# Kernel optimization log

Measured on AMD Instinct MI355X. Metric: run time of the kernel, lower is better.

## Reference

```python
import jax, jax.numpy as jnp
import numpy as np

HID = 1024
RATIO = 4          # compress_ratio
SELECT_K = 512
WINDOW = 256
N_HEADS = 16
SCALE = 1.0 / np.sqrt(HID // N_HEADS)  # 1/sqrt(head_size), head_size=64


def setup_inputs() -> dict:
    key = jax.random.key(0)
    ks = jax.random.split(key, 12)
    std = 0.02
    d = {
        "hidden_states": jax.random.normal(ks[0], (4, 4096, HID), jnp.float32),
        # torch Linear weight [out,in] stored here transposed as [in,out]
        "Wq": jax.random.normal(ks[1], (HID, HID), jnp.float32) * std,
        "bq": jnp.zeros((HID,), jnp.float32),
        "Wk": jax.random.normal(ks[2], (HID, HID), jnp.float32) * std,
        "bk": jnp.zeros((HID,), jnp.float32),
        "Wv": jax.random.normal(ks[3], (HID, HID), jnp.float32) * std,
        "bv": jnp.zeros((HID,), jnp.float32),
        "Wo": jax.random.normal(ks[4], (3 * HID, HID), jnp.float32) * std,
        "bo": jnp.zeros((HID,), jnp.float32),
        "Wg": jax.random.normal(ks[5], (HID, 3), jnp.float32) * std,
        "bg": jnp.zeros((3,), jnp.float32),
        "Wc": jax.random.normal(ks[6], (RATIO * HID, HID), jnp.float32) * std,
        "bc": jnp.zeros((HID,), jnp.float32),
        "Ws": jax.random.normal(ks[7], (HID, 1), jnp.float32) * std,
        "bs": jnp.zeros((1,), jnp.float32),
    }
    return d


def _adjust(t, L):
    cur = t.shape[1]
    if cur < L:
        return jnp.pad(t, ((0, 0), (0, L - cur), (0, 0)))
    return t[:, :L]


def _attend(x, Wq, bq, Wk, bk, Wv, bv):
    # x: [..., T, H]; full single-head attention over axis -2
    q = x @ Wq + bq
    k = x @ Wk + bk
    v = x @ Wv + bv
    s = jnp.einsum('...qd,...kd->...qk', q, k) * SCALE
    p = jax.nn.softmax(s, axis=-1)
    return jnp.einsum('...qk,...kd->...qd', p, v)


def reference(hidden_states, Wq, bq, Wk, bk, Wv, bv, Wo, bo, Wg, bg, Wc, bc, Ws, bs):
    B, L, H = hidden_states.shape

    # --- gates ---
    gates = jax.nn.sigmoid(hidden_states @ Wg + bg)
    gates = gates / (gates.sum(-1, keepdims=True) + 1e-6)

    # --- compress branch: block-compress then full attention over blocks ---
    pad_c = (-L) % RATIO
    xc = jnp.pad(hidden_states, ((0, 0), (0, pad_c), (0, 0)))
    blocks = xc.reshape(B, -1, RATIO * H)
    compressed = blocks @ Wc + bc                      # [B, Lc, H]
    comp_out = _adjust(_attend(compressed, Wq, bq, Wk, bk, Wv, bv), L)

    # --- select branch: top-k token gather then full attention ---
    k_eff = min(SELECT_K, L)
    scores = (hidden_states @ Ws + bs)[..., 0]         # [B, L]
    _, idx = jax.lax.top_k(scores, k_eff)
    idx = jnp.sort(idx, axis=-1)
    selected = jnp.take_along_axis(hidden_states, idx[..., None], axis=1)  # [B, k, H]
    sel_out = _adjust(_attend(selected, Wq, bq, Wk, bk, Wv, bv), L)

    # --- window branch: overlapping sliding windows (stride W/2) ---
    W = min(WINDOW, L)
    pad_w = (-L) % W
    xw = jnp.pad(hidden_states, ((0, 0), (0, pad_w), (0, 0)))
    Lp = xw.shape[1]
    starts = np.arange(0, Lp - W + 1, W // 2)
    widx = starts[:, None] + np.arange(W)              # [nw, W] static
    win = xw[:, widx]                                   # [B, nw, W, H]
    win_ctx = _attend(win, Wq, bq, Wk, bk, Wv, bv)      # [B, nw, W, H]
    win_out = _adjust(win_ctx.reshape(B, -1, H), L)

    # --- gated combine + output projection + residual + layernorm ---
    combined = jnp.concatenate([
        comp_out * gates[..., 0:1],
        sel_out * gates[..., 1:2],
        win_out * gates[..., 2:3],
    ], axis=-1)
    out = combined @ Wo + bo
    out = out * 0.5 + hidden_states * 0.5
    mu = out.mean(-1, keepdims=True)
    var = out.var(-1, keepdims=True)
    return (out - mu) * jax.lax.rsqrt(var + 1e-6)
```

## Files before the change

### kernel.cpp

```cpp
#include <hip/hip_runtime.h>
#include <hip/hip_bf16.h>

typedef __bf16 bf16;
typedef __bf16 bf16x4 __attribute__((ext_vector_type(4)));
typedef __bf16 bf16x8 __attribute__((ext_vector_type(8)));
typedef float floatx4 __attribute__((ext_vector_type(4)));

#define MFMA16(a, b, c) __builtin_amdgcn_mfma_f32_16x16x32_bf16((a), (b), (c), 0, 0, 0)
#define SCALE_F 0.125f

#define GLDS(gp, lp) __builtin_amdgcn_global_load_lds( \
    (const __attribute__((address_space(1))) void*)(gp), \
    (__attribute__((address_space(3))) void*)(lp), 16, 0, 0)

__global__ __launch_bounds__(256) void prep_kernel(const float* __restrict__ Wq, const float* __restrict__ Wk,
                                                   const float* __restrict__ Wv, const float* __restrict__ Wo,
                                                   const float* __restrict__ Wc,
                                                   const float* __restrict__ bq, const float* __restrict__ bk,
                                                   const float* __restrict__ bv,
                                                   bf16* __restrict__ wqkvT, bf16* __restrict__ woT,
                                                   bf16* __restrict__ wcT, float* __restrict__ bqkv) {
    const int z = blockIdx.z;
    const int tx = threadIdx.x, ty = threadIdx.y;
    if (z == 10) {
        int bid = blockIdx.y * 32 + blockIdx.x;
        if (bid < 12) {
            int i = bid * 256 + ty * 32 + tx;
            float v = (i < 1024) ? bq[i] : (i < 2048 ? bk[i - 1024] : bv[i - 2048]);
            bqkv[i] = v;
        }
        return;
    }
    __shared__ float tile[32][33];
    const float* in;
    bf16* out;
    int R;
    if (z < 3)      { in = (z == 0 ? Wq : (z == 1 ? Wk : Wv)); out = wqkvT + (size_t)z * 1048576; R = 1024; }
    else if (z < 6) { in = Wo + (size_t)(z - 3) * 1048576; out = woT + (size_t)(z - 3) * 1048576; R = 1024; }
    else            { in = Wc + (size_t)(z - 6) * 1048576; out = wcT + (z - 6) * 1024; R = 4096; }
    int bx = blockIdx.x * 32, by = blockIdx.y * 32;
#pragma unroll
    for (int i = 0; i < 32; i += 8)
        tile[ty + i][tx] = in[(size_t)(by + ty + i) * 1024 + bx + tx];
    __syncthreads();
#pragma unroll
    for (int i = 0; i < 32; i += 8)
        out[(size_t)(bx + ty + i) * R + by + tx] = (bf16)tile[tx][ty + i];
}

__global__ __launch_bounds__(256) void gates_scores_kernel(const float* __restrict__ x,
                                                           const float* __restrict__ Wg, const float* __restrict__ bg,
                                                           const float* __restrict__ Ws, const float* __restrict__ bs,
                                                           float* __restrict__ gates, float* __restrict__ scores,
                                                           bf16* __restrict__ xb) {
    int row = blockIdx.x * 4 + (threadIdx.x >> 6);
    int lane = threadIdx.x & 63;
    const float* xr = x + (size_t)row * 1024 + lane * 16;
    float g0 = 0.f, g1 = 0.f, g2 = 0.f;
    double sc = 0.0;
    bf16x8 xo0, xo1;
#pragma unroll
    for (int i = 0; i < 16; i++) {
        float xv = xr[i];
        if (i < 8) xo0[i] = (bf16)xv; else xo1[i - 8] = (bf16)xv;
        int k = lane * 16 + i;
        g0 += xv * Wg[k * 3 + 0];
        g1 += xv * Wg[k * 3 + 1];
        g2 += xv * Wg[k * 3 + 2];
        sc += (double)(xv * Ws[k]);
    }
    bf16* xbp = xb + (size_t)row * 1024 + lane * 16;
    *(bf16x8*)xbp = xo0;
    *(bf16x8*)(xbp + 8) = xo1;
    for (int off = 1; off < 64; off <<= 1) {
        g0 += __shfl_xor(g0, off);
        g1 += __shfl_xor(g1, off);
        g2 += __shfl_xor(g2, off);
        sc += __shfl_xor(sc, off);
    }
    if (lane == 0) {
        g0 = 1.0f / (1.0f + __expf(-(g0 + bg[0])));
        g1 = 1.0f / (1.0f + __expf(-(g1 + bg[1])));
        g2 = 1.0f / (1.0f + __expf(-(g2 + bg[2])));
        float den = g0 + g1 + g2 + 1e-6f;
        gates[(size_t)row * 3 + 0] = g0 / den;
        gates[(size_t)row * 3 + 1] = g1 / den;
        gates[(size_t)row * 3 + 2] = g2 / den;
        scores[row] = (float)(sc + (double)bs[0]);
    }
}

__global__ __launch_bounds__(256) void rank_kernel(const float* __restrict__ scores, int* __restrict__ rankP) {
    __shared__ float s[1024];
    const int b = blockIdx.z, jc = blockIdx.y;
    const int i = blockIdx.x * 256 + threadIdx.x;
    const float* sb = scores + b * 4096;
    ((float4*)s)[threadIdx.x] = ((const float4*)(sb + jc * 1024))[threadIdx.x];
    __syncthreads();
    const float si = sb[i];
    const int jbase = jc * 1024;
    int cnt = 0;
#pragma unroll 4
    for (int jj = 0; jj < 1024; jj += 4) {
        float4 v = *(const float4*)(s + jj);
        int j0 = jbase + jj;
        cnt += (v.x > si) || (v.x == si && (j0 + 0) < i);
        cnt += (v.y > si) || (v.y == si && (j0 + 1) < i);
        cnt += (v.z > si) || (v.z == si && (j0 + 2) < i);
        cnt += (v.w > si) || (v.w == si && (j0 + 3) < i);
    }
    rankP[jc * 16384 + b * 4096 + i] = cnt;
}

__global__ __launch_bounds__(1024) void select_kernel(const int* __restrict__ rankP, int* __restrict__ sidx) {
    __shared__ int psum[1024];
    int b = blockIdx.x, t = threadIdx.x;
    const int* rb = rankP + b * 4096;
    int f[4];
#pragma unroll
    for (int k = 0; k < 4; k++) {
        int idx = 4 * t + k;
        int r = rb[idx] + rb[16384 + idx] + rb[32768 + idx] + rb[49152 + idx];
        f[k] = r < 512;
    }
    psum[t] = f[0] + f[1] + f[2] + f[3];
    __syncthreads();
    for (int off = 1; off < 1024; off <<= 1) {
        int u = (t >= off) ? psum[t - off] : 0;
        __syncthreads();
        psum[t] += u;
        __syncthreads();
    }
    int pos = t ? psum[t - 1] : 0;
    int* ob = sidx + b * 512;
    if (f[0]) ob[pos++] = 4 * t + 0;
    if (f[1]) ob[pos++] = 4 * t + 1;
    if (f[2]) ob[pos++] = 4 * t + 2;
    if (f[3]) ob[pos++] = 4 * t + 3;
}

__global__ __launch_bounds__(256) void gather_kernel(const bf16* __restrict__ Qf, const bf16* __restrict__ Kf,
                                                     const bf16* __restrict__ Vf, const int* __restrict__ sidx,
                                                     bf16* __restrict__ sq, bf16* __restrict__ sk,
                                                     bf16* __restrict__ sv) {
    int e = blockIdx.x * 256 + threadIdx.x;
    int col = (e & 127) * 8;
    int i = (e >> 7) & 511;
    int b = e >> 16;
    int src = b * 4096 + (sidx[b * 512 + i] & 4095);
    size_t so = (size_t)src * 1024 + col;
    size_t dofs = (size_t)(b * 512 + i) * 1024 + col;
    *(float4*)(sq + dofs) = *(const float4*)(Qf + so);
    *(float4*)(sk + dofs) = *(const float4*)(Kf + so);
    *(float4*)(sv + dofs) = *(const float4*)(Vf + so);
}

__global__ __launch_bounds__(256) void addcvt4_kernel(const float* __restrict__ P0, const float* __restrict__ P1,
                                                      const float* __restrict__ P2, const float* __restrict__ P3,
                                                      const float* __restrict__ bc, bf16* __restrict__ outp) {
    int i = blockIdx.x * 256 + threadIdx.x;
    float4 a = ((const float4*)P0)[i];
    float4 b = ((const float4*)P1)[i];
    float4 c = ((const float4*)P2)[i];
    float4 d = ((const float4*)P3)[i];
    int col = (i << 2) & 1023;
    bf16x4 o;
    o[0] = (bf16)(a.x + b.x + c.x + d.x + bc[col + 0]);
    o[1] = (bf16)(a.y + b.y + c.y + d.y + bc[col + 1]);
    o[2] = (bf16)(a.z + b.z + c.z + d.z + bc[col + 2]);
    o[3] = (bf16)(a.w + b.w + c.w + d.w + bc[col + 3]);
    *(bf16x4*)(outp + ((size_t)i << 2)) = o;
}

template <bool NZF, bool F32OUT, bool ACC, bool REMAP>
__global__ __launch_bounds__(256) void gemm3(const bf16* __restrict__ A, const bf16* __restrict__ Bt,
                                             void* __restrict__ Cv, const float* __restrict__ bias, int biasz,
                                             int K, int lda, int ldb, int ldc, int zdiv,
                                             size_t sAhi, size_t sAlo, size_t sBhi, size_t sBlo,
                                             size_t sChi, size_t sClo, int mpbA, int mpbC) {
    __shared__ float4 smA[512], smB[512];
    bf16* sA = (bf16*)smA;
    bf16* sB = (bf16*)smB;
    const int t = threadIdx.x;
    const int lane = t & 63, quad = lane >> 4, l16 = lane & 15;
    const int wv = t >> 6, wm = wv >> 1, wn = wv & 1;
    const int mt = blockIdx.y;
    int nt, zh, zl;
    if constexpr (NZF) {
        zh = blockIdx.z;
        zl = blockIdx.x / zdiv;
        nt = blockIdx.x - zl * zdiv;
    } else {
        nt = blockIdx.x;
        int z = blockIdx.z;
        zh = z / zdiv;
        zl = z - zh * zdiv;
    }
    A  += (size_t)zh * sAhi + (size_t)zl * sAlo;
    Bt += (size_t)zh * sBhi + (size_t)zl * sBlo;
    const size_t cofs = (size_t)zh * sChi + (size_t)zl * sClo;

    floatx4 acc[4][4] = {};

    const bf16* Ap = A + (size_t)(mt * 128 + (t >> 2)) * lda + (t & 3) * 8;
    const bf16* Bp = Bt + (size_t)(nt * 128 + (t >> 2)) * ldb + (t & 3) * 8;
    const size_t rA = (size_t)64 * lda, rB = (size_t)64 * ldb;
    bf16* lA0 = sA + wv * 512;
    bf16* lA1 = sA + 2048 + wv * 512;
    bf16* lB0 = sB + wv * 512;
    bf16* lB1 = sB + 2048 + wv * 512;

    for (int k0 = 0; k0 < K; k0 += 32) {
        __syncthreads();
        GLDS(Ap + k0,      lA0);
        GLDS(Ap + rA + k0, lA1);
        GLDS(Bp + k0,      lB0);
        GLDS(Bp + rB + k0, lB1);
        __syncthreads();
        bf16x8 af[4], bfr[4];
#pragma unroll
        for (int i = 0; i < 4; i++) af[i] = *(const bf16x8*)(sA + (wm * 64 + i * 16 + l16) * 32 + quad * 8);
#pragma unroll
        for (int j = 0; j < 4; j++) bfr[j] = *(const bf16x8*)(sB + (wn * 64 + j * 16 + l16) * 32 + quad * 8);
#pragma unroll
        for (int i = 0; i < 4; i++)
#pragma unroll
            for (int j = 0; j < 4; j++) acc[i][j] = MFMA16(af[i], bfr[j], acc[i][j]);
    }

#pragma unroll
    for (int i = 0; i < 4; i++) {
        int gr0 = mt * 128 + wm * 64 + i * 16 + quad * 4;
#pragma unroll
        for (int j = 0; j < 4; j++) {
            int gc = nt * 128 + wn * 64 + j * 16 + l16;
            float bvl = bias ? bias[zl * biasz + gc] : 0.0f;
#pragma unroll
            for (int r = 0; r < 4; r++) {
                int row = gr0 + r;
                size_t crow = REMAP ? ((size_t)(row / mpbA) * mpbC + (row % mpbA)) : (size_t)row;
                size_t off = cofs + crow * ldc + gc;
                float v = acc[i][j][r] + bvl;
                if constexpr (F32OUT) {
                    float* Cf = (float*)Cv;
                    if constexpr (ACC) v += Cf[off];
                    Cf[off] = v;
                } else {
                    bf16* Cb = (bf16*)Cv;
                    if constexpr (ACC) v += (float)Cb[off];
                    Cb[off] = (bf16)v;
                }
            }
        }
    }
}

#define BARx()   asm volatile("s_barrier" ::: "memory")
#define LGKM0()  asm volatile("s_waitcnt lgkmcnt(0)" ::: "memory")
#define VMC6()   asm volatile("s_waitcnt vmcnt(6)" ::: "memory")

#define LD_A(bsel, qm) { \
    const bf16* _p = lds + (bsel) * 32768 + (((qm) << 7) + (wm << 6) + l16) * 64; \
    _Pragma("unroll") \
    for (int m = 0; m < 4; m++) { \
        a[m][0] = *(const bf16x8*)(_p + (m << 10) + cg0); \
        a[m][1] = *(const bf16x8*)(_p + (m << 10) + cg1); \
    } }

#define LD_B(bsel, qn) { \
    const bf16* _p = lds + (bsel) * 32768 + 16384 + (((qn) << 7) + (wn << 5) + l16) * 64; \
    _Pragma("unroll") \
    for (int n = 0; n < 2; n++) { \
        b[qn][n][0] = *(const bf16x8*)(_p + (n << 10) + cg0); \
        b[qn][n][1] = *(const bf16x8*)(_p + (n << 10) + cg1); \
    } }

#define ST_A(bsel, h, ko) { \
    bf16* _d = lds + (bsel) * 32768 + (((h) << 7) + (wv << 3)) * 64; \
    const bf16* _g = Ab + (size_t)((h) << 7) * lda + (ko); \
    GLDS(_g, _d); \
    GLDS(_g + ((size_t)lda << 6), _d + 4096); }

#define ST_B(bsel, h, ko) { \
    bf16* _d = lds + (bsel) * 32768 + 16384 + (((h) << 7) + (wv << 3)) * 64; \
    const bf16* _g = Bb + (size_t)((h) << 7) * ldb + (ko); \
    GLDS(_g, _d); \
    GLDS(_g + ((size_t)ldb << 6), _d + 4096); }

#define PH_MMA(qm, qn) { \
    __builtin_amdgcn_s_setprio(1); \
    _Pragma("unroll") \
    for (int kk = 0; kk < 2; kk++) \
    _Pragma("unroll") \
    for (int m = 0; m < 4; m++) \
    _Pragma("unroll") \
    for (int n = 0; n < 2; n++) \
        acc[qm][qn][m][n] = MFMA16(a[m][kk], b[qn][n][kk], acc[qm][qn][m][n]); \
    __builtin_amdgcn_s_setprio(0); }

template <bool NZF, bool F32OUT, bool ACC, bool REMAP>
__global__ __launch_bounds__(512, 2) void gemm256(const bf16* __restrict__ A, const bf16* __restrict__ Bt,
                                                  void* __restrict__ Cv, const float* __restrict__ bias, int biasz,
                                                  int K, int lda, int ldb, int ldc, int zdiv,
                                                  size_t sAhi, size_t sAlo, size_t sBhi, size_t sBlo,
                                                  size_t sChi, size_t sClo, int mpbA, int mpbC) {
    __shared__ float4 ldsv[8192];
    bf16* lds = (bf16*)ldsv;
    const int t = threadIdx.x;
    const int lane = t & 63, quad = lane >> 4, l16 = lane & 15;
    const int wv = t >> 6, wm = wv >> 2, wn = wv & 3;

    const int gx = gridDim.x;
    int lin = blockIdx.x + gx * blockIdx.y;
    const int chunk = (gx * gridDim.y) >> 3;
    lin = (lin & 7) * chunk + (lin >> 3);
    const int bx = lin % gx;
    const int mt = lin / gx;

    int nt, zh, zl;
    if constexpr (NZF) {
        zh = blockIdx.z;
        zl = bx / zdiv;
        nt = bx - zl * zdiv;
    } else {
        nt = bx;
        int z = blockIdx.z;
        zh = z / zdiv;
        zl = z - zh * zdiv;
    }
    A  += (size_t)zh * sAhi + (size_t)zl * sAlo;
    Bt += (size_t)zh * sBhi + (size_t)zl * sBlo;
    const size_t cofs = (size_t)zh * sChi + (size_t)zl * sClo;

    const int srow = (wv << 3) + (lane >> 3);
    const int scol = (((lane & 7) ^ ((lane >> 3) & 7)) << 3);
    const bf16* Ab = A + (size_t)(mt * 256 + srow) * lda + scol;
    const bf16* Bb = Bt + (size_t)(nt * 256 + srow) * ldb + scol;
    const int swz = l16 & 7;
    const int cg0 = ((quad ^ swz) << 3);
    const int cg1 = (((4 | quad) ^ swz) << 3);

    floatx4 acc[2][2][4][2] = {};
    bf16x8 a[4][2], b[2][2][2];

    const int NT = K >> 6;
    ST_A(0, 0, 0);  ST_B(0, 0, 0);  ST_B(0, 1, 0);  ST_A(0, 1, 0);
    ST_A(1, 0, 64); ST_B(1, 0, 64); ST_B(1, 1, 64); ST_A(1, 1, 64);
    VMC6();
    BARx();

#pragma unroll 1
    for (int it = 0; it < (NT >> 1); ++it) {
        const int kt = it << 1;
        const int ko2 = ((kt + 2 < NT) ? kt + 2 : NT - 1) << 6;
        const int ko3 = ((kt + 3 < NT) ? kt + 3 : NT - 1) << 6;
        LD_B(0, 0); LD_A(0, 0);
        PH_MMA(0, 0);
        LGKM0(); BARx();
        LD_B(0, 1);
        ST_A(0, 0, ko2);
        PH_MMA(0, 1);
        LGKM0(); BARx();
        LD_A(0, 1);
        ST_B(0, 0, ko2);
        PH_MMA(1, 1);
        LGKM0(); BARx();
        ST_B(0, 1, ko2);
        PH_MMA(1, 0);
        VMC6(); BARx();
        LD_B(1, 0); LD_A(1, 0);
        ST_A(0, 1, ko2);
        PH_MMA(0, 0);
        LGKM0(); BARx();
        LD_B(1, 1);
        ST_A(1, 0, ko3);
        PH_MMA(0, 1);
        LGKM0(); BARx();
        LD_A(1, 1);
        ST_B(1, 0, ko3);
        PH_MMA(1, 1);
        LGKM0(); BARx();
        ST_B(1, 1, ko3);
        ST_A(1, 1, ko3);
        PH_MMA(1, 0);
        VMC6(); BARx();
    }

    asm volatile("s_waitcnt vmcnt(0)" ::: "memory");
    BARx();

    if constexpr (!ACC && !REMAP) {
        const int STE = F32OUT ? 260 : 264;
        float* ldsf = (float*)ldsv;
        bf16* ldsh = (bf16*)ldsv;
#pragma unroll
        for (int qm = 0; qm < 2; qm++)
#pragma unroll
        for (int mh = 0; mh < 2; mh++) {
#pragma unroll
            for (int qn = 0; qn < 2; qn++)
#pragma unroll
            for (int n = 0; n < 2; n++) {
                const int ccol = qn * 128 + wn * 32 + n * 16 + l16;
                const float bvl = bias ? bias[zl * biasz + nt * 256 + ccol] : 0.0f;
#pragma unroll
                for (int mp = 0; mp < 2; mp++) {
                    const int lr0 = wm * 32 + mp * 16 + quad * 4;
#pragma unroll
                    for (int r = 0; r < 4; r++) {
                        float v = acc[qm][qn][mh * 2 + mp][n][r] + bvl;
                        if constexpr (F32OUT) ldsf[(lr0 + r) * STE + ccol] = v;
                        else                  ldsh[(lr0 + r) * STE + ccol] = (bf16)v;
                    }
                }
            }
            LGKM0(); BARx();
            if constexpr (F32OUT) {
                float* Cf = (float*)Cv;
#pragma unroll
                for (int i = 0; i < 8; i++) {
                    int idx = i * 512 + t;
                    int row = idx >> 6, c4 = (idx & 63) << 2;
                    float4 vv = *(float4*)(ldsf + row * STE + c4);
                    int grow = mt * 256 + qm * 128 + ((row >> 5) << 6) + mh * 32 + (row & 31);
                    *(float4*)(Cf + cofs + (size_t)grow * ldc + nt * 256 + c4) = vv;
                }
            } else {
                bf16* Cb = (bf16*)Cv;
#pragma unroll
                for (int i = 0; i < 4; i++) {
                    int idx = i * 512 + t;
                    int row = idx >> 5, c8 = (idx & 31) << 3;
                    float4 vv = *(float4*)(ldsh + row * STE + c8);
                    int grow = mt * 256 + qm * 128 + ((row >> 5) << 6) + mh * 32 + (row & 31);
                    *(float4*)(Cb + cofs + (size_t)grow * ldc + nt * 256 + c8) = vv;
                }
            }
            LGKM0(); BARx();
        }
    } else {
#pragma unroll
        for (int qm = 0; qm < 2; qm++)
#pragma unroll
        for (int m = 0; m < 4; m++) {
            int gr0 = mt * 256 + qm * 128 + wm * 64 + m * 16 + quad * 4;
#pragma unroll
            for (int qn = 0; qn < 2; qn++)
#pragma unroll
            for (int n = 0; n < 2; n++) {
                int gc = nt * 256 + qn * 128 + wn * 32 + n * 16 + l16;
                float bvl = bias ? bias[zl * biasz + gc] : 0.0f;
#pragma unroll
                for (int r = 0; r < 4; r++) {
                    int row = gr0 + r;
                    size_t crow = REMAP ? ((size_t)(row / mpbA) * mpbC + (row % mpbA)) : (size_t)row;
                    size_t off = cofs + crow * ldc + gc;
                    float v = acc[qm][qn][m][n][r] + bvl;
                    if constexpr (F32OUT) {
                        float* Cf = (float*)Cv;
                        if constexpr (ACC) v += Cf[off];
                        Cf[off] = v;
                    } else {
                        bf16* Cb = (bf16*)Cv;
                        if constexpr (ACC) v += (float)Cb[off];
                        Cb[off] = (bf16)v;
                    }
                }
            }
        }
    }
}

#undef LD_A
#undef LD_B
#undef ST_A
#undef ST_B
#undef PH_MMA

template <int MODE>
__global__ __launch_bounds__(256) void smtb_kernel(const float* __restrict__ S, bf16* __restrict__ P,
                                                   const float* __restrict__ gates, int RL,
                                                   int upb, int wbase, int nsm,
                                                   const bf16* __restrict__ tin, bf16* __restrict__ tout,
                                                   int TR, int TC) {
    __shared__ float red[8];
    __shared__ bf16 tile[32][33];
    const int t = threadIdx.x;
    if ((int)blockIdx.x >= nsm) {
        int tb = blockIdx.x - nsm;
        int bx = (tb & 31) * 32, by = (tb >> 5) * 32;
        int tx = t & 31, ty = t >> 5;
#pragma unroll
        for (int i = 0; i < 32; i += 8)
            tile[ty + i][tx] = tin[(size_t)(by + ty + i) * TC + bx + tx];
        __syncthreads();
#pragma unroll
        for (int i = 0; i < 32; i += 8)
            tout[(size_t)(bx + ty + i) * TR + by + tx] = tile[tx][ty + i];
        return;
    }
    const int row = blockIdx.x;
    const float* srow = S + (size_t)row * RL;
    bf16* prow = P + (size_t)row * RL;
    const int npt = RL >> 8;
    float v[4];
    float m = -1e30f;
    for (int i = 0; i < npt; i++) { v[i] = srow[t + (i << 8)] * SCALE_F; m = fmaxf(m, v[i]); }
    for (int off = 1; off < 64; off <<= 1) m = fmaxf(m, __shfl_xor(m, off));
    const int wvv = t >> 6, lane = t & 63;
    if (lane == 0) red[wvv] = m;
    __syncthreads();
    m = fmaxf(fmaxf(red[0], red[1]), fmaxf(red[2], red[3]));
    float e[4], s = 0.f;
    for (int i = 0; i < npt; i++) { e[i] = __expf(v[i] - m); s += e[i]; }
    for (int off = 1; off < 64; off <<= 1) s += __shfl_xor(s, off);
    if (lane == 0) red[4 + wvv] = s;
    __syncthreads();
    s = red[4] + red[5] + red[6] + red[7];
    int gpos;
    if (MODE == 0)      { gpos = (row >> 10) * 4096 + (row & 1023); }
    else if (MODE == 1) { gpos = (row >> 9) * 4096 + (row & 511); }
    else                { int zz = row >> 8; gpos = (zz / upb) * 4096 + (wbase + zz % upb) * 256 + (row & 255); }
    const float fac = gates[gpos * 3 + MODE] / s;
    for (int i = 0; i < npt; i++) prow[t + (i << 8)] = (bf16)(e[i] * fac);
}

__global__ __launch_bounds__(256) void ln_kernel(float* __restrict__ acc, const float* __restrict__ x) {
    __shared__ float red[8];
    int row = blockIdx.x, t = threadIdx.x;
    float4 a = ((const float4*)(acc + (size_t)row * 1024))[t];
    float4 xv = ((const float4*)(x + (size_t)row * 1024))[t];
    float y[4];
    y[0] = 0.5f * a.x + 0.5f * xv.x;
    y[1] = 0.5f * a.y + 0.5f * xv.y;
    y[2] = 0.5f * a.z + 0.5f * xv.z;
    y[3] = 0.5f * a.w + 0.5f * xv.w;
    float s = 0.f, s2 = 0.f;
#pragma unroll
    for (int i = 0; i < 4; i++) { s += y[i]; s2 += y[i] * y[i]; }
    for (int off = 1; off < 64; off <<= 1) { s += __shfl_xor(s, off); s2 += __shfl_xor(s2, off); }
    int wvv = t >> 6, lane = t & 63;
    if (lane == 0) { red[wvv] = s; red[4 + wvv] = s2; }
    __syncthreads();
    s = red[0] + red[1] + red[2] + red[3];
    s2 = red[4] + red[5] + red[6] + red[7];
    float mu = s * (1.0f / 1024.0f);
    float var = s2 * (1.0f / 1024.0f) - mu * mu;
    float rs = rsqrtf(var + 1e-6f);
    float4 o;
    o.x = (y[0] - mu) * rs;
    o.y = (y[1] - mu) * rs;
    o.z = (y[2] - mu) * rs;
    o.w = (y[3] - mu) * rs;
    ((float4*)(acc + (size_t)row * 1024))[t] = o;
}

extern "C" void kernel_launch(void* const* d_in, const int* in_sizes, int n_in,
                              void* d_out, int out_size, void* d_ws, size_t ws_size,
                              hipStream_t stream) {
    (void)in_sizes; (void)n_in; (void)out_size; (void)ws_size;
    const float* x  = (const float*)d_in[0];
    const float* Wq = (const float*)d_in[1];
    const float* bq = (const float*)d_in[2];
    const float* Wk = (const float*)d_in[3];
    const float* bk = (const float*)d_in[4];
    const float* Wv = (const float*)d_in[5];
    const float* bv = (const float*)d_in[6];
    const float* Wo = (const float*)d_in[7];
    const float* bo = (const float*)d_in[8];
    const float* Wg = (const float*)d_in[9];
    const float* bg = (const float*)d_in[10];
    const float* Wc = (const float*)d_in[11];
    const float* bc = (const float*)d_in[12];
    const float* Ws = (const float*)d_in[13];
    const float* bs = (const float*)d_in[14];
    float* out = (float*)d_out;

    char* w = (char*)d_ws;
    const size_t MB = 1024 * 1024;
    bf16* xb    = (bf16*)(w + 0 * MB);
    bf16* Pwin  = (bf16*)(w + 0 * MB);
    bf16* cq    = (bf16*)(w + 0 * MB);
    bf16* ck    = (bf16*)(w + 8 * MB);
    bf16* cv    = (bf16*)(w + 16 * MB);
    bf16* Pcomp = (bf16*)(w + 24 * MB);
    float* Ssel = (float*)(w + 0 * MB);
    bf16* Psel  = (bf16*)(w + 4 * MB);
    bf16* sel_o = (bf16*)(w + 6 * MB);
    bf16* qf    = (bf16*)(w + 32 * MB);
    bf16* vfT   = (bf16*)(w + 32 * MB);
    bf16* kf    = (bf16*)(w + 64 * MB);
    bf16* win_o = (bf16*)(w + 64 * MB);
    bf16* vf    = (bf16*)(w + 96 * MB);
    bf16* comp  = (bf16*)(w + 128 * MB);
    float* compP = (float*)(w + 32 * MB);
    int* rankP = (int*)(w + 96 * MB);
    bf16* cvT = (bf16*)(w + 96 * MB);
    float* Swin  = (float*)(w + 136 * MB);
    float* Scomp = (float*)(w + 136 * MB);
    bf16* comp_o = (bf16*)(w + 144 * MB);
    bf16* wqkvT = (bf16*)(w + 152 * MB);
    bf16* wcT   = (bf16*)(w + 158 * MB);
    bf16* woT0  = (bf16*)(w + 166 * MB);
    bf16* woT1  = (bf16*)(w + 168 * MB);
    bf16* woT2  = (bf16*)(w + 170 * MB);
    bf16* sq    = (bf16*)(w + 172 * MB);
    bf16* sk    = (bf16*)(w + 176 * MB);
    bf16* sv    = (bf16*)(w + 180 * MB);
    bf16* svT   = (bf16*)(w + 184 * MB);
    float* bqkv    = (float*)(w + 188 * MB);
    float* gatesF  = bqkv + 3072;
    float* scoresF = gatesF + 49152;
    int*   sidx    = (int*)(scoresF + 16384);

    dim3 tb(32, 8);

    gates_scores_kernel<<<4096, 256, 0, stream>>>(x, Wg, bg, Ws, bs, gatesF, scoresF, xb);
    prep_kernel<<<dim3(32, 32, 11), tb, 0, stream>>>(Wq, Wk, Wv, Wo, Wc, bq, bk, bv, wqkvT, woT0, wcT, bqkv);
    rank_kernel<<<dim3(16, 4, 4), 256, 0, stream>>>(scoresF, rankP);
    select_kernel<<<4, 1024, 0, stream>>>(rankP, sidx);

    gemm256<false,true,false,false><<<dim3(4, 16, 4), 512, 0, stream>>>(
        xb, wcT, compP, nullptr, 0, 1024, 4096, 4096, 1024, 1,
        (size_t)1024, 0, (size_t)1024, 0, (size_t)4194304, 0, 1, 1);
    addcvt4_kernel<<<4096, 256, 0, stream>>>(compP, compP + (size_t)4194304,
                                             compP + (size_t)8388608, compP + (size_t)12582912, bc, comp);

    gemm256<true,false,false,false><<<dim3(12, 64, 1), 512, 0, stream>>>(
        xb, wqkvT, qf, bqkv, 1024, 1024, 1024, 1024, 1024, 4,
        0, 0, 0, (size_t)1048576, 0, (size_t)16777216, 1, 1);

    gather_kernel<<<1024, 256, 0, stream>>>(qf, kf, vf, sidx, sq, sk, sv);

    gemm3<false,true,false,false><<<dim3(2, 2, 64), 256, 0, stream>>>(
        qf, kf, Swin, nullptr, 0, 1024, 1024, 1024, 256, 16,
        (size_t)4194304, (size_t)131072, (size_t)4194304, (size_t)131072, (size_t)1048576, (size_t)65536, 1, 1);
    smtb_kernel<2><<<32768, 256, 0, stream>>>(Swin, Pwin, gatesF, 256, 16, 0, 16384, vf, vfT, 16384, 1024);
    gemm3<false,false,false,false><<<dim3(8, 2, 64), 256, 0, stream>>>(
        Pwin, vfT, win_o, nullptr, 0, 256, 256, 16384, 1024, 16,
        (size_t)1048576, (size_t)65536, (size_t)4096, (size_t)128, (size_t)4194304, (size_t)262144, 1, 1);
    gemm256<false,true,false,false><<<dim3(4, 64, 1), 512, 0, stream>>>(
        win_o, woT2, out, bo, 0, 1024, 1024, 1024, 1024, 1, 0, 0, 0, 0, 0, 0, 1, 1);

    gemm256<true,false,false,false><<<dim3(12, 16, 1), 512, 0, stream>>>(
        comp, wqkvT, cq, bqkv, 1024, 1024, 1024, 1024, 1024, 4,
        0, 0, 0, (size_t)1048576, 0, (size_t)4194304, 1, 1);
    gemm3<false,true,false,false><<<dim3(8, 8, 4), 256, 0, stream>>>(
        cq, ck, Scomp, nullptr, 0, 1024, 1024, 1024, 1024, 1,
        (size_t)1048576, 0, (size_t)1048576, 0, (size_t)1048576, 0, 1, 1);
    smtb_kernel<0><<<8192, 256, 0, stream>>>(Scomp, Pcomp, gatesF, 1024, 0, 0, 4096, cv, cvT, 4096, 1024);
    gemm3<false,false,false,false><<<dim3(8, 8, 4), 256, 0, stream>>>(
        Pcomp, cvT, comp_o, nullptr, 0, 1024, 1024, 4096, 1024, 1,
        (size_t)1048576, 0, (size_t)1024, 0, (size_t)1048576, 0, 1, 1);
    gemm3<false,true,true,true><<<dim3(8, 32, 1), 256, 0, stream>>>(
        comp_o, woT0, out, nullptr, 0, 1024, 1024, 1024, 1024, 1, 0, 0, 0, 0, 0, 0, 1024, 4096);

    gemm3<false,true,false,false><<<dim3(4, 4, 4), 256, 0, stream>>>(
        sq, sk, Ssel, nullptr, 0, 1024, 1024, 1024, 512, 1,
        (size_t)524288, 0, (size_t)524288, 0, (size_t)262144, 0, 1, 1);
    smtb_kernel<1><<<4096, 256, 0, stream>>>(Ssel, Psel, gatesF, 512, 0, 0, 2048, sv, svT, 2048, 1024);
    gemm3<false,false,false,false><<<dim3(8, 4, 4), 256, 0, stream>>>(
        Psel, svT, sel_o, nullptr, 0, 512, 512, 2048, 1024, 1,
        (size_t)262144, 0, (size_t)512, 0, (size_t)524288, 0, 1, 1);
    gemm3<false,true,true,true><<<dim3(8, 16, 1), 256, 0, stream>>>(
        sel_o, woT1, out, nullptr, 0, 1024, 1024, 1024, 1024, 1, 0, 0, 0, 0, 0, 0, 512, 4096);

    ln_kernel<<<16384, 256, 0, stream>>>(out, x);
}
```

Baseline: 770.8 us.

## Batch compress and select attention GEMMs and softmax into shared launches

Merges the independent compress-branch and select-branch attention stages into combined launches: one grouped kernel for both QK^T products, one for both softmax+transpose passes, and one for both PV products. The select scores move to a separate buffer so the two branches no longer alias. This removes launch overhead and fills the GPU better, since each small branch GEMM alone uses few workgroups. The cost is some idle blocks that exit early in the padded grid, plus more branching in the kernels.

```diff
diff --git a/kernel.cpp b/kernel.cpp
--- a/kernel.cpp
+++ b/kernel.cpp
@@ -172,30 +172,16 @@
     *(bf16x4*)(outp + ((size_t)i << 2)) = o;
 }
 
-template <bool NZF, bool F32OUT, bool ACC, bool REMAP>
-__global__ __launch_bounds__(256) void gemm3(const bf16* __restrict__ A, const bf16* __restrict__ Bt,
-                                             void* __restrict__ Cv, const float* __restrict__ bias, int biasz,
-                                             int K, int lda, int ldb, int ldc, int zdiv,
-                                             size_t sAhi, size_t sAlo, size_t sBhi, size_t sBlo,
-                                             size_t sChi, size_t sClo, int mpbA, int mpbC) {
-    __shared__ float4 smA[512], smB[512];
-    bf16* sA = (bf16*)smA;
-    bf16* sB = (bf16*)smB;
+template <bool F32OUT, bool ACC, bool REMAP>
+__device__ __forceinline__ void gemm3_body(int nt, int mt, int zh, int zl, bf16* sA, bf16* sB,
+                                           const bf16* __restrict__ A, const bf16* __restrict__ Bt,
+                                           void* __restrict__ Cv, const float* __restrict__ bias, int biasz,
+                                           int K, int lda, int ldb, int ldc,
+                                           size_t sAhi, size_t sAlo, size_t sBhi, size_t sBlo,
+                                           size_t sChi, size_t sClo, int mpbA, int mpbC) {
     const int t = threadIdx.x;
     const int lane = t & 63, quad = lane >> 4, l16 = lane & 15;
     const int wv = t >> 6, wm = wv >> 1, wn = wv & 1;
-    const int mt = blockIdx.y;
-    int nt, zh, zl;
-    if constexpr (NZF) {
-        zh = blockIdx.z;
-        zl = blockIdx.x / zdiv;
-        nt = blockIdx.x - zl * zdiv;
-    } else {
-        nt = blockIdx.x;
-        int z = blockIdx.z;
-        zh = z / zdiv;
-        zl = z - zh * zdiv;
-    }
     A  += (size_t)zh * sAhi + (size_t)zl * sAlo;
     Bt += (size_t)zh * sBhi + (size_t)zl * sBlo;
     const size_t cofs = (size_t)zh * sChi + (size_t)zl * sClo;
@@ -252,6 +238,49 @@
                 }
             }
         }
+    }
+}
+
+template <bool NZF, bool F32OUT, bool ACC, bool REMAP>
+__global__ __launch_bounds__(256) void gemm3(const bf16* __restrict__ A, const bf16* __restrict__ Bt,
+                                             void* __restrict__ Cv, const float* __restrict__ bias, int biasz,
+                                             int K, int lda, int ldb, int ldc, int zdiv,
+                                             size_t sAhi, size_t sAlo, size_t sBhi, size_t sBlo,
+                                             size_t sChi, size_t sClo, int mpbA, int mpbC) {
+    __shared__ float4 smA[512], smB[512];
+    const int mt = blockIdx.y;
+    int nt, zh, zl;
+    if constexpr (NZF) {
+        zh = blockIdx.z;
+        zl = blockIdx.x / zdiv;
+        nt = blockIdx.x - zl * zdiv;
+    } else {
+        nt = blockIdx.x;
+        int z = blockIdx.z;
+        zh = z / zdiv;
+        zl = z - zh * zdiv;
+    }
+    gemm3_body<F32OUT, ACC, REMAP>(nt, mt, zh, zl, (bf16*)smA, (bf16*)smB,
+                                   A, Bt, Cv, bias, biasz, K, lda, ldb, ldc,
+                                   sAhi, sAlo, sBhi, sBlo, sChi, sClo, mpbA, mpbC);
+}
+
+template <bool F32OUT>
+__global__ __launch_bounds__(256) void gemm3_pair(int nzA, int nxB, int nyB,
+        const bf16* __restrict__ A1, const bf16* __restrict__ B1, void* __restrict__ C1,
+        int K1, int lda1, int ldb1, int ldc1, size_t sAhi1, size_t sBhi1, size_t sChi1,
+        const bf16* __restrict__ A2, const bf16* __restrict__ B2, void* __restrict__ C2,
+        int K2, int lda2, int ldb2, int ldc2, size_t sAhi2, size_t sBhi2, size_t sChi2) {
+    __shared__ float4 smA[512], smB[512];
+    if ((int)blockIdx.z < nzA) {
+        gemm3_body<F32OUT, false, false>(blockIdx.x, blockIdx.y, blockIdx.z, 0, (bf16*)smA, (bf16*)smB,
+                                         A1, B1, C1, nullptr, 0, K1, lda1, ldb1, ldc1,
+                                         sAhi1, 0, sBhi1, 0, sChi1, 0, 1, 1);
+    } else {
+        if ((int)blockIdx.x >= nxB || (int)blockIdx.y >= nyB) return;
+        gemm3_body<F32OUT, false, false>(blockIdx.x, blockIdx.y, blockIdx.z - nzA, 0, (bf16*)smA, (bf16*)smB,
+                                         A2, B2, C2, nullptr, 0, K2, lda2, ldb2, ldc2,
+                                         sAhi2, 0, sBhi2, 0, sChi2, 0, 1, 1);
     }
 }
 
@@ -477,32 +506,9 @@
 #undef ST_B
 #undef PH_MMA
 
-template <int MODE>
-__global__ __launch_bounds__(256) void smtb_kernel(const float* __restrict__ S, bf16* __restrict__ P,
-                                                   const float* __restrict__ gates, int RL,
-                                                   int upb, int wbase, int nsm,
-                                                   const bf16* __restrict__ tin, bf16* __restrict__ tout,
-                                                   int TR, int TC) {
-    __shared__ float red[8];
-    __shared__ bf16 tile[32][33];
+__device__ __forceinline__ void sm_body(const float* __restrict__ srow, bf16* __restrict__ prow,
+                                        int npt, float gate, float* red) {
     const int t = threadIdx.x;
-    if ((int)blockIdx.x >= nsm) {
-        int tb = blockIdx.x - nsm;
-        int bx = (tb & 31) * 32, by = (tb >> 5) * 32;
-        int tx = t & 31, ty = t >> 5;
-#pragma unroll
-        for (int i = 0; i < 32; i += 8)
-            tile[ty + i][tx] = tin[(size_t)(by + ty + i) * TC + bx + tx];
-        __syncthreads();
-#pragma unroll
-        for (int i = 0; i < 32; i += 8)
-            tout[(size_t)(bx + ty + i) * TR + by + tx] = tile[tx][ty + i];
-        return;
-    }
-    const int row = blockIdx.x;
-    const float* srow = S + (size_t)row * RL;
-    bf16* prow = P + (size_t)row * RL;
-    const int npt = RL >> 8;
     float v[4];
     float m = -1e30f;
     for (int i = 0; i < npt; i++) { v[i] = srow[t + (i << 8)] * SCALE_F; m = fmaxf(m, v[i]); }
@@ -517,12 +523,59 @@
     if (lane == 0) red[4 + wvv] = s;
     __syncthreads();
     s = red[4] + red[5] + red[6] + red[7];
-    int gpos;
-    if (MODE == 0)      { gpos = (row >> 10) * 4096 + (row & 1023); }
-    else if (MODE == 1) { gpos = (row >> 9) * 4096 + (row & 511); }
-    else                { int zz = row >> 8; gpos = (zz / upb) * 4096 + (wbase + zz % upb) * 256 + (row & 255); }
-    const float fac = gates[gpos * 3 + MODE] / s;
+    const float fac = gate / s;
     for (int i = 0; i < npt; i++) prow[t + (i << 8)] = (bf16)(e[i] * fac);
+}
+
+__device__ __forceinline__ void tp_body(const bf16* __restrict__ tin, bf16* __restrict__ tout,
+                                        int TR, int TC, int tb, bf16 (*tile)[33]) {
+    const int t = threadIdx.x;
+    int bx = (tb & 31) * 32, by = (tb >> 5) * 32;
+    int tx = t & 31, ty = t >> 5;
+#pragma unroll
+    for (int i = 0; i < 32; i += 8)
+        tile[ty + i][tx] = tin[(size_t)(by + ty + i) * TC + bx + tx];
+    __syncthreads();
+#pragma unroll
+    for (int i = 0; i < 32; i += 8)
+        tout[(size_t)(bx + ty + i) * TR + by + tx] = tile[tx][ty + i];
+}
+
+__global__ __launch_bounds__(256) void smtb_win_kernel(const float* __restrict__ S, bf16* __restrict__ P,
+                                                       const float* __restrict__ gates, int nsm,
+                                                       const bf16* __restrict__ tin, bf16* __restrict__ tout) {
+    __shared__ float red[8];
+    __shared__ bf16 tile[32][33];
+    if ((int)blockIdx.x >= nsm) {
+        tp_body(tin, tout, 16384, 1024, blockIdx.x - nsm, tile);
+        return;
+    }
+    const int row = blockIdx.x;
+    int zz = row >> 8;
+    int gpos = (zz / 16) * 4096 + (zz % 16) * 256 + (row & 255);
+    sm_body(S + (size_t)row * 256, P + (size_t)row * 256, 1, gates[gpos * 3 + 2], red);
+}
+
+__global__ __launch_bounds__(256) void smtb2_kernel(const float* __restrict__ S0, bf16* __restrict__ P0,
+                                                    const float* __restrict__ S1, bf16* __restrict__ P1,
+                                                    const float* __restrict__ gates,
+                                                    const bf16* __restrict__ cv, bf16* __restrict__ cvT,
+                                                    const bf16* __restrict__ sv, bf16* __restrict__ svT) {
+    __shared__ float red[8];
+    __shared__ bf16 tile[32][33];
+    const int i = blockIdx.x;
+    if (i < 4096) {
+        int gpos = (i >> 10) * 4096 + (i & 1023);
+        sm_body(S0 + (size_t)i * 1024, P0 + (size_t)i * 1024, 4, gates[gpos * 3 + 0], red);
+    } else if (i < 8192) {
+        tp_body(cv, cvT, 4096, 1024, i - 4096, tile);
+    } else if (i < 10240) {
+        int row = i - 8192;
+        int gpos = (row >> 9) * 4096 + (row & 511);
+        sm_body(S1 + (size_t)row * 512, P1 + (size_t)row * 512, 2, gates[gpos * 3 + 1], red);
+    } else {
+        tp_body(sv, svT, 2048, 1024, i - 10240, tile);
+    }
 }
 
 __global__ __launch_bounds__(256) void ln_kernel(float* __restrict__ acc, const float* __restrict__ x) {
@@ -584,7 +637,6 @@
     bf16* ck    = (bf16*)(w + 8 * MB);
     bf16* cv    = (bf16*)(w + 16 * MB);
     bf16* Pcomp = (bf16*)(w + 24 * MB);
-    float* Ssel = (float*)(w + 0 * MB);
     bf16* Psel  = (bf16*)(w + 4 * MB);
     bf16* sel_o = (bf16*)(w + 6 * MB);
     bf16* qf    = (bf16*)(w + 32 * MB);
@@ -596,6 +648,7 @@
     float* compP = (float*)(w + 32 * MB);
     int* rankP = (int*)(w + 96 * MB);
     bf16* cvT = (bf16*)(w + 96 * MB);
+    float* SselN = (float*)(w + 104 * MB);
     float* Swin  = (float*)(w + 136 * MB);
     float* Scomp = (float*)(w + 136 * MB);
     bf16* comp_o = (bf16*)(w + 144 * MB);
@@ -635,7 +688,7 @@
     gemm3<false,true,false,false><<<dim3(2, 2, 64), 256, 0, stream>>>(
         qf, kf, Swin, nullptr, 0, 1024, 1024, 1024, 256, 16,
         (size_t)4194304, (size_t)131072, (size_t)4194304, (size_t)131072, (size_t)1048576, (size_t)65536, 1, 1);
-    smtb_kernel<2><<<32768, 256, 0, stream>>>(Swin, Pwin, gatesF, 256, 16, 0, 16384, vf, vfT, 16384, 1024);
+    smtb_win_kernel<<<32768, 256, 0, stream>>>(Swin, Pwin, gatesF, 16384, vf, vfT);
     gemm3<false,false,false,false><<<dim3(8, 2, 64), 256, 0, stream>>>(
         Pwin, vfT, win_o, nullptr, 0, 256, 256, 16384, 1024, 16,
         (size_t)1048576, (size_t)65536, (size_t)4096, (size_t)128, (size_t)4194304, (size_t)262144, 1, 1);
@@ -645,23 +698,19 @@
     gemm256<true,false,false,false><<<dim3(12, 16, 1), 512, 0, stream>>>(
         comp, wqkvT, cq, bqkv, 1024, 1024, 1024, 1024, 1024, 4,
         0, 0, 0, (size_t)1048576, 0, (size_t)4194304, 1, 1);
-    gemm3<false,true,false,false><<<dim3(8, 8, 4), 256, 0, stream>>>(
-        cq, ck, Scomp, nullptr, 0, 1024, 1024, 1024, 1024, 1,
-        (size_t)1048576, 0, (size_t)1048576, 0, (size_t)1048576, 0, 1, 1);
-    smtb_kernel<0><<<8192, 256, 0, stream>>>(Scomp, Pcomp, gatesF, 1024, 0, 0, 4096, cv, cvT, 4096, 1024);
-    gemm3<false,false,false,false><<<dim3(8, 8, 4), 256, 0, stream>>>(
-        Pcomp, cvT, comp_o, nullptr, 0, 1024, 1024, 4096, 1024, 1,
-        (size_t)1048576, 0, (size_t)1024, 0, (size_t)1048576, 0, 1, 1);
+
+    gemm3_pair<true><<<dim3(8, 8, 8), 256, 0, stream>>>(4, 4, 4,
+        cq, ck, Scomp, 1024, 1024, 1024, 1024, (size_t)1048576, (size_t)1048576, (size_t)1048576,
+        sq, sk, SselN, 1024, 1024, 1024, 512, (size_t)524288, (size_t)524288, (size_t)262144);
+
+    smtb2_kernel<<<12288, 256, 0, stream>>>(Scomp, Pcomp, SselN, Psel, gatesF, cv, cvT, sv, svT);
+
+    gemm3_pair<false><<<dim3(8, 8, 8), 256, 0, stream>>>(4, 8, 4,
+        Pcomp, cvT, comp_o, 1024, 1024, 4096, 1024, (size_t)1048576, (size_t)1024, (size_t)1048576,
+        Psel, svT, sel_o, 512, 512, 2048, 1024, (size_t)262144, (size_t)512, (size_t)524288);
+
     gemm3<false,true,true,true><<<dim3(8, 32, 1), 256, 0, stream>>>(
         comp_o, woT0, out, nullptr, 0, 1024, 1024, 1024, 1024, 1, 0, 0, 0, 0, 0, 0, 1024, 4096);
-
-    gemm3<false,true,false,false><<<dim3(4, 4, 4), 256, 0, stream>>>(
-        sq, sk, Ssel, nullptr, 0, 1024, 1024, 1024, 512, 1,
-        (size_t)524288, 0, (size_t)524288, 0, (size_t)262144, 0, 1, 1);
-    smtb_kernel<1><<<4096, 256, 0, stream>>>(Ssel, Psel, gatesF, 512, 0, 0, 2048, sv, svT, 2048, 1024);
-    gemm3<false,false,false,false><<<dim3(8, 4, 4), 256, 0, stream>>>(
-        Psel, svT, sel_o, nullptr, 0, 512, 512, 2048, 1024, 1,
-        (size_t)262144, 0, (size_t)512, 0, (size_t)524288, 0, 1, 1);
     gemm3<false,true,true,true><<<dim3(8, 16, 1), 256, 0, stream>>>(
         sel_o, woT1, out, nullptr, 0, 1024, 1024, 1024, 1024, 1, 0, 0, 0, 0, 0, 0, 512, 4096);
 
```

Measured after the change: 733.7 us. 4.8% less time.
